# Optimization experiments

Hardware: AMD Instinct MI355X
Metric: run time of the kernel (lower is better)

The kernel has to match this reference:

```python
import jax, jax.numpy as jnp
import numpy as np

B, S, D = 4, 2048, 512
H = 8
DK = D // H  # 64, dim_q = dim_k
DFF = 2048
EPS = 1e-5


def _layernorm(x, g, b):
    mu = jnp.mean(x, axis=-1, keepdims=True)
    var = jnp.var(x, axis=-1, keepdims=True)
    return (x - mu) * jax.lax.rsqrt(var + EPS) * g + b


def setup_inputs() -> dict:
    key = jax.random.key(0)
    ks = jax.random.split(key, 12)
    s = 0.02
    return {
        "src": jax.random.normal(ks[0], (B, S, D), jnp.float32),
        "mask": jnp.ones((B, S, S), jnp.int32),
        # per-head projections (stacked over heads, faithful to separate Linear layers)
        "q_w": jax.random.normal(ks[1], (H, D, DK), jnp.float32) * s,
        "q_b": jnp.zeros((H, DK), jnp.float32),
        "k_w": jax.random.normal(ks[2], (H, D, DK), jnp.float32) * s,
        "k_b": jnp.zeros((H, DK), jnp.float32),
        "v_w": jax.random.normal(ks[3], (H, D, DK), jnp.float32) * s,
        "v_b": jnp.zeros((H, DK), jnp.float32),
        "o_w": jax.random.normal(ks[4], (H * DK, D), jnp.float32) * s,
        "o_b": jnp.zeros((D,), jnp.float32),
        "ln1_g": jnp.ones((D,), jnp.float32),
        "ln1_b": jnp.zeros((D,), jnp.float32),
        "w1": jax.random.normal(ks[5], (D, DFF), jnp.float32) * s,
        "b1": jnp.zeros((DFF,), jnp.float32),
        "w2": jax.random.normal(ks[6], (DFF, D), jnp.float32) * s,
        "b2": jnp.zeros((D,), jnp.float32),
        "ln2_g": jnp.ones((D,), jnp.float32),
        "ln2_b": jnp.zeros((D,), jnp.float32),
    }


def reference(src, mask, q_w, q_b, k_w, k_b, v_w, v_b, o_w, o_b,
              ln1_g, ln1_b, w1, b1, w2, b2, ln2_g, ln2_b):
    # --- multi-head self-attention (all heads vectorized) ---
    q = jnp.einsum('bsd,hde->bhse', src, q_w) + q_b[None, :, None, :]
    k = jnp.einsum('bsd,hde->bhse', src, k_w) + k_b[None, :, None, :]
    v = jnp.einsum('bsd,hde->bhse', src, v_w) + v_b[None, :, None, :]
    scores = jnp.einsum('bhqe,bhke->bhqk', q, k)  # [B,H,S,S]
    scores = jnp.where(mask[:, None, :, :] == 0, jnp.float32(-1e20), scores)
    scale = jnp.float32(DK) ** 0.5
    attn = jax.nn.softmax(scores / scale, axis=-1)
    ctx = jnp.einsum('bhqk,bhke->bhqe', attn, v)  # [B,H,S,DK]
    ctx = ctx.transpose(0, 2, 1, 3).reshape(B, S, H * DK)  # concat heads
    attn_out = ctx @ o_w + o_b
    x = _layernorm(src + attn_out, ln1_g, ln1_b)
    # --- feed forward ---
    ff = jax.nn.relu(x @ w1 + b1) @ w2 + b2
    return _layernorm(x + ff, ln2_g, ln2_b)
```

## Files before the change

kernel.cpp:

```cpp
#include <hip/hip_runtime.h>


typedef __bf16 bf16x8 __attribute__((ext_vector_type(8)));
typedef float f32x4 __attribute__((ext_vector_type(4)));
typedef unsigned short us4 __attribute__((ext_vector_type(4)));
typedef unsigned u32x4 __attribute__((ext_vector_type(4)));

__device__ __forceinline__ unsigned short f2bf(float f){
  unsigned u = __builtin_bit_cast(unsigned, f);
  u += 0x7fffu + ((u >> 16) & 1u);
  return (unsigned short)(u >> 16);
}

__device__ __forceinline__ unsigned cvt_pk_bf16(float lo, float hi){
  unsigned r;
  asm("v_cvt_pk_bf16_f32 %0, %1, %2" : "=v"(r) : "v"(lo), "v"(hi));
  return r;
}
__device__ __forceinline__ void plswap32(unsigned &a, unsigned &b){
  asm volatile("v_permlane32_swap_b32 %0, %1" : "+v"(a), "+v"(b));
}
__device__ __forceinline__ void plswap16(unsigned &a, unsigned &b){
  asm volatile("v_permlane16_swap_b32 %0, %1" : "+v"(a), "+v"(b));
}
__device__ __forceinline__ float exp2_hw(float x){
  float r;
  asm("v_exp_f32 %0, %1" : "=v"(r) : "v"(x));
  return r;
}

typedef const __attribute__((address_space(1))) void* gas_t;
typedef __attribute__((address_space(3))) void* las_t;
__device__ __forceinline__ void gl_lds16(const void* g, void* l){
  __builtin_amdgcn_global_load_lds((gas_t)g, (las_t)l, 16, 0, 0);
}

struct PrepSh { float t[32][33]; unsigned red[4]; };

__device__ __forceinline__ void wtrans_body(const float* __restrict__ in,
    unsigned short* __restrict__ out, int K, int N, int k0, int n0, int tid,
    float (*t)[33]){
  int tx = tid & 31, ty = tid >> 5;
  #pragma unroll
  for (int r = 0; r < 4; ++r)
    t[ty + 8*r][tx] = in[(size_t)(k0 + ty + 8*r)*N + n0 + tx];
  __syncthreads();
  #pragma unroll
  for (int r = 0; r < 4; ++r)
    out[(size_t)(n0 + ty + 8*r)*K + k0 + tx] = f2bf(t[tx][ty + 8*r]);
}

__global__ __launch_bounds__(256) void k_prep(
    const int* __restrict__ mask, const float* __restrict__ src,
    const float* __restrict__ qw, const float* __restrict__ kw, const float* __restrict__ vw,
    const float* __restrict__ qb, const float* __restrict__ kb, const float* __restrict__ vb,
    const float* __restrict__ ow, const float* __restrict__ w1, const float* __restrict__ w2,
    unsigned short* __restrict__ mb16, unsigned short* __restrict__ x_bf,
    unsigned short* __restrict__ wtqkv, float* __restrict__ bqkv,
    unsigned short* __restrict__ wto, unsigned short* __restrict__ wt1,
    unsigned short* __restrict__ wt2)
{
  __shared__ PrepSh sh;
  const int tid = threadIdx.x;
  int id = blockIdx.x;
  if (id < 256){
    const int bq = id & 127, half = id >> 7;
    const int b = bq >> 5, qt = bq & 31;
    const int* base = mask + (size_t)b*2048*2048 + (size_t)(qt*64 + (tid>>4)*4)*2048 + (tid&15)*4;
    unsigned bits = 0;
    for (int i = 0; i < 16; ++i){
      const int* p = base + (half*16 + i)*64;
      int ok = 1;
      #pragma unroll
      for (int r = 0; r < 4; ++r){
        int4 v = *reinterpret_cast<const int4*>(p + (size_t)r*2048);
        ok &= (v.x!=0)&(v.y!=0)&(v.z!=0)&(v.w!=0);
      }
      bits |= (unsigned)ok << i;
    }
    #pragma unroll
    for (int o = 1; o < 64; o <<= 1) bits &= __shfl_xor(bits, o);
    if ((tid & 63) == 0) sh.red[tid >> 6] = bits;
    __syncthreads();
    if (tid == 0) mb16[bq*2 + half] = (unsigned short)(sh.red[0]&sh.red[1]&sh.red[2]&sh.red[3]);
    return;
  }
  id -= 256;
  if (id < 4096){
    int i = id * 256 + tid;
    float4 v = reinterpret_cast<const float4*>(src)[i];
    us4 o = { f2bf(v.x), f2bf(v.y), f2bf(v.z), f2bf(v.w) };
    reinterpret_cast<us4*>(x_bf)[i] = o;
    return;
  }
  id -= 4096;
  if (id < 768){
    int z = id / 32, rem = id % 32, x = rem & 15, y = rem >> 4;
    int sel = z >> 3, h = z & 7;
    const float* in = (sel==0 ? qw : (sel==1 ? kw : vw)) + (size_t)h*512*64;
    unsigned short* o = wtqkv + ((size_t)(sel*512 + h*64)) * 512;
    wtrans_body(in, o, 512, 64, x*32, y*32, tid, sh.t);
    return;
  }
  id -= 768;
  if (id < 6){
    int n = id*256 + tid;
    if (n < 1536){ int sel = n >> 9, r = n & 511;
      bqkv[n] = (sel==0 ? qb : (sel==1 ? kb : vb))[r]; }
    return;
  }
  id -= 6;
  if (id < 256){
    wtrans_body(ow, wto, 512, 512, (id & 15)*32, (id >> 4)*32, tid, sh.t);
    return;
  }
  id -= 256;
  if (id < 1024){
    wtrans_body(w1, wt1, 512, 2048, (id & 15)*32, (id >> 4)*32, tid, sh.t);
    return;
  }
  id -= 1024;
  wtrans_body(w2, wt2, 2048, 512, (id & 63)*32, (id >> 6)*32, tid, sh.t);
}

template<int MODE>
__global__ __launch_bounds__(256, 3) void k_gemm(
    const unsigned short* __restrict__ A, const unsigned short* __restrict__ Bt,
    const float* __restrict__ bias, const float* __restrict__ resid,
    unsigned short* __restrict__ ob0, unsigned short* __restrict__ ob1, unsigned short* __restrict__ ob2,
    float* __restrict__ of, int M, int N, int K)
{
  __shared__ unsigned short As[128*64];
  __shared__ unsigned short Bs[128*64];
  const int tid = threadIdx.x, lane = tid & 63, wid = tid >> 6;
  const int g = lane >> 4, lr = lane & 15;
  const int rowBase = blockIdx.x * 128, colBase = blockIdx.y * 128;
  const int wr = (wid >> 1) * 64, wc = (wid & 1) * 64;
  const int srow8 = lane >> 3;
  const int schunk = (lane & 7) ^ (srow8 & 7);
  const unsigned short* pA = A + (size_t)(rowBase + wid*32 + srow8)*K + schunk*8;
  const unsigned short* pB = Bt + (size_t)(colBase + wid*32 + srow8)*K + schunk*8;
  f32x4 acc[4][4] = {};
  for (int k0 = 0; k0 < K; k0 += 64){
    __syncthreads();
    #pragma unroll
    for (int t = 0; t < 4; ++t){
      gl_lds16(pA + (size_t)(t*8)*K + k0, &As[(wid*32 + t*8)*64]);
      gl_lds16(pB + (size_t)(t*8)*K + k0, &Bs[(wid*32 + t*8)*64]);
    }
    __syncthreads();
    #pragma unroll
    for (int ks = 0; ks < 2; ++ks){
      const int rc = ((ks*4 + g) ^ (lr & 7)) * 8;
      bf16x8 af[4], bfr[4];
      #pragma unroll
      for (int mi = 0; mi < 4; ++mi) af[mi]  = *reinterpret_cast<const bf16x8*>(&As[(wr + mi*16 + lr)*64 + rc]);
      #pragma unroll
      for (int ni = 0; ni < 4; ++ni) bfr[ni] = *reinterpret_cast<const bf16x8*>(&Bs[(wc + ni*16 + lr)*64 + rc]);
      __builtin_amdgcn_s_setprio(1);
      #pragma unroll
      for (int mi = 0; mi < 4; ++mi)
        #pragma unroll
        for (int ni = 0; ni < 4; ++ni)
          acc[mi][ni] = __builtin_amdgcn_mfma_f32_16x16x32_bf16(af[mi], bfr[ni], acc[mi][ni], 0, 0, 0);
      __builtin_amdgcn_s_setprio(0);
    }
  }
  float bv[4];
  #pragma unroll
  for (int ni = 0; ni < 4; ++ni) bv[ni] = bias[colBase + wc + ni*16 + lr];
  #pragma unroll
  for (int mi = 0; mi < 4; ++mi){
    #pragma unroll
    for (int ni = 0; ni < 4; ++ni){
      #pragma unroll
      for (int j = 0; j < 4; ++j){
        int m = rowBase + wr + mi*16 + g*4 + j;
        int n = colBase + wc + ni*16 + lr;
        float v = acc[mi][ni][j] + bv[ni];
        if constexpr (MODE == 0){
          int b = m >> 11, s = m & 2047;
          int sel = n >> 9, rr = n & 511, h = rr >> 6, e = rr & 63;
          size_t bh = (size_t)(b*8 + h);
          if (sel == 0)      ob0[(bh*2048 + s)*64 + e] = f2bf(v);
          else if (sel == 1) ob1[(bh*2048 + s)*64 + e] = f2bf(v);
          else               ob2[(bh*64 + e)*2048 + s] = f2bf(v);
        } else if constexpr (MODE == 1 || MODE == 3){
          of[(size_t)m*N + n] = v + resid[(size_t)m*N + n];
        } else {
          ob0[(size_t)m*N + n] = f2bf(v > 0.f ? v : 0.f);
        }
      }
    }
  }
}

__global__ __launch_bounds__(512) void k_attn(
    const unsigned short* __restrict__ Qb, const unsigned short* __restrict__ Kb,
    const unsigned short* __restrict__ Vt, const int* __restrict__ mask,
    const unsigned* __restrict__ mbits_p, unsigned short* __restrict__ ctx)
{
  __shared__ unsigned short Ks[2][4096];
  __shared__ unsigned short Vs[2][4096];
  const int tid = threadIdx.x, lane = tid & 63, wid = tid >> 6;
  const int g = lane >> 4, lr = lane & 15;
  const int qt = blockIdx.y, bh = blockIdx.x;
  const int b = bh >> 3, h = bh & 7;
  const int qw = qt * 128 + wid * 16;
  const unsigned mbits = mbits_p[b*32 + qt*2] & mbits_p[b*32 + qt*2 + 1];
  const size_t mbase = (size_t)b * 2048 * 2048;
  const float SC = 0.18033688f;

  const int srow8 = lane >> 3;
  const int schunk = (lane & 7) ^ (srow8 & 7);
  const unsigned short* kgb = Kb + (size_t)bh*2048*64 + ((size_t)(wid*8) + srow8)*64 + schunk*8;
  const unsigned short* vgb = Vt + (size_t)bh*64*2048 + ((size_t)(wid*8) + srow8)*2048 + schunk*8;

  #define STAGE(buf, t) do { \
    gl_lds16(kgb + (size_t)(t)*4096, &Ks[buf][(wid*8)*64]); \
    gl_lds16(vgb + (size_t)(t)*64,   &Vs[buf][(wid*8)*64]); \
  } while(0)

  STAGE(0, 0);

  bf16x8 b_q[2];
  {
    const unsigned short* qp = Qb + ((size_t)bh*2048 + qw + lr)*64;
    b_q[0] = *reinterpret_cast<const bf16x8*>(qp + g*8);
    b_q[1] = *reinterpret_cast<const bf16x8*>(qp + 32 + g*8);
  }
  f32x4 acc[4] = {};
  float m_run = -3.0e38f, lp = 0.f;
  int cur = 0;
  __syncthreads();

  for (int kt = 0; kt < 32; ++kt){
    if (kt < 31) STAGE(cur^1, kt+1);
    const unsigned short* Kc = Ks[cur];
    const unsigned short* Vc = Vs[cur];
    f32x4 st[4] = {};
    __builtin_amdgcn_s_setprio(1);
    #pragma unroll
    for (int mk = 0; mk < 4; ++mk)
      #pragma unroll
      for (int ks = 0; ks < 2; ++ks){
        bf16x8 kf = *reinterpret_cast<const bf16x8*>(
            &Kc[(mk*16 + lr)*64 + (((ks*4 + g) ^ (lr & 7)))*8]);
        st[mk] = __builtin_amdgcn_mfma_f32_16x16x32_bf16(kf, b_q[ks], st[mk], 0,0,0);
      }
    __builtin_amdgcn_s_setprio(0);
    if (!((mbits >> kt) & 1)){
      const int kk0 = kt * 64;
      #pragma unroll
      for (int mk = 0; mk < 4; ++mk)
        #pragma unroll
        for (int j = 0; j < 4; ++j){
          int kg = kk0 + mk*16 + g*4 + j;
          if (mask[mbase + (size_t)(qw + lr)*2048 + kg] == 0) st[mk][j] = -3.0e30f;
        }
    }
    float x0 = fmaxf(fmaxf(st[0][0], st[0][1]), st[0][2]);
    float x1 = fmaxf(fmaxf(st[0][3], st[1][0]), st[1][1]);
    float x2 = fmaxf(fmaxf(st[1][2], st[1][3]), st[2][0]);
    float x3 = fmaxf(fmaxf(st[2][1], st[2][2]), st[2][3]);
    float x4 = fmaxf(fmaxf(st[3][0], st[3][1]), st[3][2]);
    float tm = fmaxf(fmaxf(fmaxf(x0, x1), x2), fmaxf(fmaxf(x3, x4), st[3][3]));
    tm = fmaxf(tm, __shfl_xor(tm, 16));
    tm = fmaxf(tm, __shfl_xor(tm, 32));
    float tms = tm * SC;
    if (!__all(tms <= m_run + 8.f)){
      float mnew = fmaxf(m_run, tms);
      float alpha = exp2_hw(m_run - mnew);
      lp *= alpha;
      #pragma unroll
      for (int ne = 0; ne < 4; ++ne)
        #pragma unroll
        for (int j = 0; j < 4; ++j) acc[ne][j] *= alpha;
      m_run = mnew;
    }
    unsigned wrd[4][2];
    float psA = 0.f, psB = 0.f;
    #pragma unroll
    for (int mk = 0; mk < 4; ++mk){
      float p0 = exp2_hw(__builtin_fmaf(st[mk][0], SC, -m_run));
      float p1 = exp2_hw(__builtin_fmaf(st[mk][1], SC, -m_run));
      float p2 = exp2_hw(__builtin_fmaf(st[mk][2], SC, -m_run));
      float p3 = exp2_hw(__builtin_fmaf(st[mk][3], SC, -m_run));
      psA += p0 + p2; psB += p1 + p3;
      wrd[mk][0] = cvt_pk_bf16(p0, p1);
      wrd[mk][1] = cvt_pk_bf16(p2, p3);
    }
    lp += psA + psB;
    bf16x8 pw[2];
    #pragma unroll
    for (int ks = 0; ks < 2; ++ks){
      unsigned a0w = wrd[2*ks][0], b0w = wrd[2*ks+1][0];
      unsigned a1w = wrd[2*ks][1], b1w = wrd[2*ks+1][1];
      plswap32(a0w, b0w); plswap16(a0w, b0w);
      plswap32(a1w, b1w); plswap16(a1w, b1w);
      u32x4 pk = { a0w, a1w, b0w, b1w };
      pw[ks] = __builtin_bit_cast(bf16x8, pk);
    }
    __builtin_amdgcn_s_setprio(1);
    #pragma unroll
    for (int ks = 0; ks < 2; ++ks)
      #pragma unroll
      for (int ne = 0; ne < 4; ++ne){
        bf16x8 vf = *reinterpret_cast<const bf16x8*>(
            &Vc[(ne*16 + lr)*64 + (((ks*4 + g) ^ (lr & 7)))*8]);
        acc[ne] = __builtin_amdgcn_mfma_f32_16x16x32_bf16(vf, pw[ks], acc[ne], 0,0,0);
      }
    __builtin_amdgcn_s_setprio(0);
    if (kt < 31){
      __syncthreads();
      cur ^= 1;
    }
  }
  #undef STAGE
  float l = lp;
  l += __shfl_xor(l, 16);
  l += __shfl_xor(l, 32);
  float inv = 1.f / l;
  int q = qw + lr;
  #pragma unroll
  for (int ne = 0; ne < 4; ++ne){
    uint2 ow;
    ow.x = cvt_pk_bf16(acc[ne][0]*inv, acc[ne][1]*inv);
    ow.y = cvt_pk_bf16(acc[ne][2]*inv, acc[ne][3]*inv);
    *reinterpret_cast<uint2*>(&ctx[((size_t)b*2048 + q)*512 + h*64 + ne*16 + g*4]) = ow;
  }
}

__global__ __launch_bounds__(256) void k_ln(
    const float* __restrict__ in, const float* __restrict__ gma, const float* __restrict__ bta,
    float* __restrict__ of, unsigned short* __restrict__ ob)
{
  const int lane = threadIdx.x & 63, wid = threadIdx.x >> 6;
  const size_t row = (size_t)blockIdx.x * 4 + wid;
  const float* x = in + row * 512;
  const int e0 = lane * 8;
  float xv[8];
  *reinterpret_cast<float4*>(&xv[0]) = *reinterpret_cast<const float4*>(x + e0);
  *reinterpret_cast<float4*>(&xv[4]) = *reinterpret_cast<const float4*>(x + e0 + 4);
  float s = 0.f, ss = 0.f;
  #pragma unroll
  for (int i = 0; i < 8; ++i){ s += xv[i]; ss += xv[i]*xv[i]; }
  #pragma unroll
  for (int o = 1; o < 64; o <<= 1){ s += __shfl_xor(s, o); ss += __shfl_xor(ss, o); }
  float mu = s * (1.f/512.f);
  float var = ss * (1.f/512.f) - mu*mu;
  float rs = rsqrtf(var + 1e-5f);
  float gv[8], bv[8], y[8];
  *reinterpret_cast<float4*>(&gv[0]) = *reinterpret_cast<const float4*>(gma + e0);
  *reinterpret_cast<float4*>(&gv[4]) = *reinterpret_cast<const float4*>(gma + e0 + 4);
  *reinterpret_cast<float4*>(&bv[0]) = *reinterpret_cast<const float4*>(bta + e0);
  *reinterpret_cast<float4*>(&bv[4]) = *reinterpret_cast<const float4*>(bta + e0 + 4);
  #pragma unroll
  for (int i = 0; i < 8; ++i) y[i] = (xv[i]-mu)*rs*gv[i] + bv[i];
  *reinterpret_cast<float4*>(of + row*512 + e0)     = *reinterpret_cast<float4*>(&y[0]);
  *reinterpret_cast<float4*>(of + row*512 + e0 + 4) = *reinterpret_cast<float4*>(&y[4]);
  if (ob){
    us4 o0 = { f2bf(y[0]), f2bf(y[1]), f2bf(y[2]), f2bf(y[3]) };
    us4 o1 = { f2bf(y[4]), f2bf(y[5]), f2bf(y[6]), f2bf(y[7]) };
    *reinterpret_cast<us4*>(ob + row*512 + e0)     = o0;
    *reinterpret_cast<us4*>(ob + row*512 + e0 + 4) = o1;
  }
}

extern "C" void kernel_launch(void* const* d_in, const int* in_sizes, int n_in,
                              void* d_out, int out_size, void* d_ws, size_t ws_size,
                              hipStream_t stream)
{
  const float* src  = (const float*)d_in[0];
  const int*   mask = (const int*)d_in[1];
  const float* q_w  = (const float*)d_in[2];
  const float* q_b  = (const float*)d_in[3];
  const float* k_w  = (const float*)d_in[4];
  const float* k_b  = (const float*)d_in[5];
  const float* v_w  = (const float*)d_in[6];
  const float* v_b  = (const float*)d_in[7];
  const float* o_w  = (const float*)d_in[8];
  const float* o_b  = (const float*)d_in[9];
  const float* ln1g = (const float*)d_in[10];
  const float* ln1b = (const float*)d_in[11];
  const float* w1   = (const float*)d_in[12];
  const float* b1   = (const float*)d_in[13];
  const float* w2   = (const float*)d_in[14];
  const float* b2   = (const float*)d_in[15];
  const float* ln2g = (const float*)d_in[16];
  const float* ln2b = (const float*)d_in[17];

  char* ws = (char*)d_ws;
  if (ws_size < 81795072) return;
  unsigned short* x_bf  = (unsigned short*)(ws + 0);
  unsigned short* wtqkv = (unsigned short*)(ws + 8388608);
  float*          bqkv  = (float*)(ws + 9961472);
  unsigned short* wto   = (unsigned short*)(ws + 9967616);
  unsigned short* wt1   = (unsigned short*)(ws + 10491904);
  unsigned short* wt2   = (unsigned short*)(ws + 12589056);
  unsigned short* Qb    = (unsigned short*)(ws + 14686208);
  unsigned short* Kb    = (unsigned short*)(ws + 23074816);
  unsigned short* Vt    = (unsigned short*)(ws + 31463424);
  unsigned short* ctx   = (unsigned short*)(ws + 39852032);
  unsigned short* ffb   = (unsigned short*)(ws + 14686208);
  float* res = (float*)(ws + 48240640);
  float* xf  = (float*)(ws + 65017856);
  unsigned short* mb16 = (unsigned short*)(ws + 48240640);
  const unsigned* mb32 = (const unsigned*)(ws + 48240640);
  float* outf = (float*)d_out;

  k_prep<<<7430, 256, 0, stream>>>(mask, src, q_w, k_w, v_w, q_b, k_b, v_b,
                                   o_w, w1, w2, mb16, x_bf, wtqkv, bqkv, wto, wt1, wt2);

  k_gemm<0><<<dim3(64,12), 256, 0, stream>>>(x_bf, wtqkv, bqkv, nullptr,
                                             Qb, Kb, Vt, nullptr, 8192, 1536, 512);
  k_attn<<<dim3(32,16), 512, 0, stream>>>(Qb, Kb, Vt, mask, mb32, ctx);
  k_gemm<1><<<dim3(64,4), 256, 0, stream>>>(ctx, wto, o_b, src,
                                            nullptr, nullptr, nullptr, res, 8192, 512, 512);
  k_ln<<<2048, 256, 0, stream>>>(res, ln1g, ln1b, xf, x_bf);
  k_gemm<2><<<dim3(64,16), 256, 0, stream>>>(x_bf, wt1, b1, nullptr,
                                             ffb, nullptr, nullptr, nullptr, 8192, 2048, 512);
  k_gemm<3><<<dim3(64,4), 256, 0, stream>>>(ffb, wt2, b2, xf,
                                            nullptr, nullptr, nullptr, res, 8192, 512, 2048);
  k_ln<<<2048, 256, 0, stream>>>(res, ln2g, ln2b, outf, nullptr);
}
```

Measured before the change: 177.9 us.

## Double attention key tile to 128 and use bf16 residual for FFN output

Measured after the change: 174.3 us. 1.02x faster.

```diff
diff --git a/kernel.cpp b/kernel.cpp
--- a/kernel.cpp
+++ b/kernel.cpp
@@ -10,6 +10,9 @@
   unsigned u = __builtin_bit_cast(unsigned, f);
   u += 0x7fffu + ((u >> 16) & 1u);
   return (unsigned short)(u >> 16);
+}
+__device__ __forceinline__ float bf2f(unsigned short s){
+  return __builtin_bit_cast(float, (unsigned)s << 16);
 }
 
 __device__ __forceinline__ unsigned cvt_pk_bf16(float lo, float hi){
@@ -127,7 +130,8 @@
 __global__ __launch_bounds__(256, 3) void k_gemm(
     const unsigned short* __restrict__ A, const unsigned short* __restrict__ Bt,
     const float* __restrict__ bias, const float* __restrict__ resid,
-    unsigned short* __restrict__ ob0, unsigned short* __restrict__ ob1, unsigned short* __restrict__ ob2,
+    unsigned short* __restrict__ ob0, const unsigned short* __restrict__ ob1,
+    unsigned short* __restrict__ ob2,
     float* __restrict__ of, int M, int N, int K)
 {
   __shared__ unsigned short As[128*64];
@@ -183,10 +187,12 @@
           int sel = n >> 9, rr = n & 511, h = rr >> 6, e = rr & 63;
           size_t bh = (size_t)(b*8 + h);
           if (sel == 0)      ob0[(bh*2048 + s)*64 + e] = f2bf(v);
-          else if (sel == 1) ob1[(bh*2048 + s)*64 + e] = f2bf(v);
+          else if (sel == 1) ((unsigned short*)ob1)[(bh*2048 + s)*64 + e] = f2bf(v);
           else               ob2[(bh*64 + e)*2048 + s] = f2bf(v);
-        } else if constexpr (MODE == 1 || MODE == 3){
+        } else if constexpr (MODE == 1){
           of[(size_t)m*N + n] = v + resid[(size_t)m*N + n];
+        } else if constexpr (MODE == 3){
+          of[(size_t)m*N + n] = v + bf2f(ob1[(size_t)m*N + n]);
         } else {
           ob0[(size_t)m*N + n] = f2bf(v > 0.f ? v : 0.f);
         }
@@ -200,8 +206,8 @@
     const unsigned short* __restrict__ Vt, const int* __restrict__ mask,
     const unsigned* __restrict__ mbits_p, unsigned short* __restrict__ ctx)
 {
-  __shared__ unsigned short Ks[2][4096];
-  __shared__ unsigned short Vs[2][4096];
+  __shared__ unsigned short Ks[2][8192];
+  __shared__ unsigned short Vs[2][8192];
   const int tid = threadIdx.x, lane = tid & 63, wid = tid >> 6;
   const int g = lane >> 4, lr = lane & 15;
   const int qt = blockIdx.y, bh = blockIdx.x;
@@ -211,14 +217,17 @@
   const size_t mbase = (size_t)b * 2048 * 2048;
   const float SC = 0.18033688f;
 
-  const int srow8 = lane >> 3;
-  const int schunk = (lane & 7) ^ (srow8 & 7);
-  const unsigned short* kgb = Kb + (size_t)bh*2048*64 + ((size_t)(wid*8) + srow8)*64 + schunk*8;
-  const unsigned short* vgb = Vt + (size_t)bh*64*2048 + ((size_t)(wid*8) + srow8)*2048 + schunk*8;
+  const int l8 = lane >> 3, l7 = lane & 7, l16 = lane >> 4, l15 = lane & 15;
+  const unsigned short* kg0 = Kb + (size_t)bh*2048*64 + ((size_t)(wid*16) + l8)*64 + ((l7 ^ (l8 & 7)))*8;
+  const int vrow0 = wid*8 + l16, vrow1 = wid*8 + 4 + l16;
+  const unsigned short* vg0 = Vt + (size_t)bh*64*2048 + (size_t)vrow0*2048 + ((l15 ^ (vrow0 & 15)))*8;
+  const unsigned short* vg1 = Vt + (size_t)bh*64*2048 + (size_t)vrow1*2048 + ((l15 ^ (vrow1 & 15)))*8;
 
   #define STAGE(buf, t) do { \
-    gl_lds16(kgb + (size_t)(t)*4096, &Ks[buf][(wid*8)*64]); \
-    gl_lds16(vgb + (size_t)(t)*64,   &Vs[buf][(wid*8)*64]); \
+    gl_lds16(kg0 + (size_t)(t)*8192,       &Ks[buf][(wid*16)*64]);    \
+    gl_lds16(kg0 + (size_t)(t)*8192 + 512, &Ks[buf][(wid*16+8)*64]);  \
+    gl_lds16(vg0 + (size_t)(t)*128,        &Vs[buf][(wid*8)*128]);    \
+    gl_lds16(vg1 + (size_t)(t)*128,        &Vs[buf][(wid*8+4)*128]);  \
   } while(0)
 
   STAGE(0, 0);
@@ -234,14 +243,16 @@
   int cur = 0;
   __syncthreads();
 
-  for (int kt = 0; kt < 32; ++kt){
-    if (kt < 31) STAGE(cur^1, kt+1);
+  for (int kt = 0; kt < 16; ++kt){
+    if (kt < 15) STAGE(cur^1, kt+1);
     const unsigned short* Kc = Ks[cur];
     const unsigned short* Vc = Vs[cur];
-    f32x4 st[4] = {};
+    f32x4 st[8];
+    #pragma unroll
+    for (int mk = 0; mk < 8; ++mk) st[mk] = f32x4{0.f,0.f,0.f,0.f};
     __builtin_amdgcn_s_setprio(1);
     #pragma unroll
-    for (int mk = 0; mk < 4; ++mk)
+    for (int mk = 0; mk < 8; ++mk)
       #pragma unroll
       for (int ks = 0; ks < 2; ++ks){
         bf16x8 kf = *reinterpret_cast<const bf16x8*>(
@@ -249,22 +260,23 @@
         st[mk] = __builtin_amdgcn_mfma_f32_16x16x32_bf16(kf, b_q[ks], st[mk], 0,0,0);
       }
     __builtin_amdgcn_s_setprio(0);
-    if (!((mbits >> kt) & 1)){
-      const int kk0 = kt * 64;
-      #pragma unroll
-      for (int mk = 0; mk < 4; ++mk)
+    if (((mbits >> (kt*2)) & 3u) != 3u){
+      const int kk0 = kt * 128;
+      #pragma unroll
+      for (int mk = 0; mk < 8; ++mk)
         #pragma unroll
         for (int j = 0; j < 4; ++j){
           int kg = kk0 + mk*16 + g*4 + j;
           if (mask[mbase + (size_t)(qw + lr)*2048 + kg] == 0) st[mk][j] = -3.0e30f;
         }
     }
-    float x0 = fmaxf(fmaxf(st[0][0], st[0][1]), st[0][2]);
-    float x1 = fmaxf(fmaxf(st[0][3], st[1][0]), st[1][1]);
-    float x2 = fmaxf(fmaxf(st[1][2], st[1][3]), st[2][0]);
-    float x3 = fmaxf(fmaxf(st[2][1], st[2][2]), st[2][3]);
-    float x4 = fmaxf(fmaxf(st[3][0], st[3][1]), st[3][2]);
-    float tm = fmaxf(fmaxf(fmaxf(x0, x1), x2), fmaxf(fmaxf(x3, x4), st[3][3]));
+    float pm[8];
+    #pragma unroll
+    for (int mk = 0; mk < 8; ++mk)
+      pm[mk] = fmaxf(fmaxf(st[mk][0], st[mk][1]), fmaxf(st[mk][2], st[mk][3]));
+    float tA = fmaxf(fmaxf(pm[0], pm[1]), fmaxf(pm[2], pm[3]));
+    float tB = fmaxf(fmaxf(pm[4], pm[5]), fmaxf(pm[6], pm[7]));
+    float tm = fmaxf(tA, tB);
     tm = fmaxf(tm, __shfl_xor(tm, 16));
     tm = fmaxf(tm, __shfl_xor(tm, 32));
     float tms = tm * SC;
@@ -278,10 +290,10 @@
         for (int j = 0; j < 4; ++j) acc[ne][j] *= alpha;
       m_run = mnew;
     }
-    unsigned wrd[4][2];
+    unsigned wrd[8][2];
     float psA = 0.f, psB = 0.f;
     #pragma unroll
-    for (int mk = 0; mk < 4; ++mk){
+    for (int mk = 0; mk < 8; ++mk){
       float p0 = exp2_hw(__builtin_fmaf(st[mk][0], SC, -m_run));
       float p1 = exp2_hw(__builtin_fmaf(st[mk][1], SC, -m_run));
       float p2 = exp2_hw(__builtin_fmaf(st[mk][2], SC, -m_run));
@@ -291,9 +303,9 @@
       wrd[mk][1] = cvt_pk_bf16(p2, p3);
     }
     lp += psA + psB;
-    bf16x8 pw[2];
-    #pragma unroll
-    for (int ks = 0; ks < 2; ++ks){
+    bf16x8 pw[4];
+    #pragma unroll
+    for (int ks = 0; ks < 4; ++ks){
       unsigned a0w = wrd[2*ks][0], b0w = wrd[2*ks+1][0];
       unsigned a1w = wrd[2*ks][1], b1w = wrd[2*ks+1][1];
       plswap32(a0w, b0w); plswap16(a0w, b0w);
@@ -303,15 +315,15 @@
     }
     __builtin_amdgcn_s_setprio(1);
     #pragma unroll
-    for (int ks = 0; ks < 2; ++ks)
+    for (int ks = 0; ks < 4; ++ks)
       #pragma unroll
       for (int ne = 0; ne < 4; ++ne){
         bf16x8 vf = *reinterpret_cast<const bf16x8*>(
-            &Vc[(ne*16 + lr)*64 + (((ks*4 + g) ^ (lr & 7)))*8]);
+            &Vc[(ne*16 + lr)*128 + (((ks*4 + g) ^ lr))*8]);
         acc[ne] = __builtin_amdgcn_mfma_f32_16x16x32_bf16(vf, pw[ks], acc[ne], 0,0,0);
       }
     __builtin_amdgcn_s_setprio(0);
-    if (kt < 31){
+    if (kt < 15){
       __syncthreads();
       cur ^= 1;
     }
@@ -357,8 +369,10 @@
   *reinterpret_cast<float4*>(&bv[4]) = *reinterpret_cast<const float4*>(bta + e0 + 4);
   #pragma unroll
   for (int i = 0; i < 8; ++i) y[i] = (xv[i]-mu)*rs*gv[i] + bv[i];
-  *reinterpret_cast<float4*>(of + row*512 + e0)     = *reinterpret_cast<float4*>(&y[0]);
-  *reinterpret_cast<float4*>(of + row*512 + e0 + 4) = *reinterpret_cast<float4*>(&y[4]);
+  if (of){
+    *reinterpret_cast<float4*>(of + row*512 + e0)     = *reinterpret_cast<float4*>(&y[0]);
+    *reinterpret_cast<float4*>(of + row*512 + e0 + 4) = *reinterpret_cast<float4*>(&y[4]);
+  }
   if (ob){
     us4 o0 = { f2bf(y[0]), f2bf(y[1]), f2bf(y[2]), f2bf(y[3]) };
     us4 o1 = { f2bf(y[4]), f2bf(y[5]), f2bf(y[6]), f2bf(y[7]) };
@@ -404,7 +418,6 @@
   unsigned short* ctx   = (unsigned short*)(ws + 39852032);
   unsigned short* ffb   = (unsigned short*)(ws + 14686208);
   float* res = (float*)(ws + 48240640);
-  float* xf  = (float*)(ws + 65017856);
   unsigned short* mb16 = (unsigned short*)(ws + 48240640);
   const unsigned* mb32 = (const unsigned*)(ws + 48240640);
   float* outf = (float*)d_out;
@@ -417,10 +430,10 @@
   k_attn<<<dim3(32,16), 512, 0, stream>>>(Qb, Kb, Vt, mask, mb32, ctx);
   k_gemm<1><<<dim3(64,4), 256, 0, stream>>>(ctx, wto, o_b, src,
                                             nullptr, nullptr, nullptr, res, 8192, 512, 512);
-  k_ln<<<2048, 256, 0, stream>>>(res, ln1g, ln1b, xf, x_bf);
+  k_ln<<<2048, 256, 0, stream>>>(res, ln1g, ln1b, nullptr, x_bf);
   k_gemm<2><<<dim3(64,16), 256, 0, stream>>>(x_bf, wt1, b1, nullptr,
                                              ffb, nullptr, nullptr, nullptr, 8192, 2048, 512);
-  k_gemm<3><<<dim3(64,4), 256, 0, stream>>>(ffb, wt2, b2, xf,
-                                            nullptr, nullptr, nullptr, res, 8192, 512, 2048);
+  k_gemm<3><<<dim3(64,4), 256, 0, stream>>>(ffb, wt2, b2, nullptr,
+                                            nullptr, x_bf, nullptr, res, 8192, 512, 2048);
   k_ln<<<2048, 256, 0, stream>>>(res, ln2g, ln2b, outf, nullptr);
 }
```
